# Optimization experiments

Measured on AMD Instinct MI355X. Metric: run time of the kernel, lower is better.

## Reference

```python
import jax, jax.numpy as jnp
import numpy as np
from jax import lax

B, H, W, C = 16, 32, 32, 256
HEADS = 8
HD = C // HEADS          # attention_head_dim = 32
KSZ = 3                  # conv_kernel_size
DIL = 2                  # dilation_rate
SCALE = HD ** -0.5


def setup_inputs() -> dict:
    key = jax.random.key(0)
    k0, k1, k2, k3 = jax.random.split(key, 4)
    return {
        "query": jax.random.normal(k0, (B, H, W, C), jnp.float32),
        "key_in": jax.random.normal(k1, (B, H, W, C), jnp.float32),
        "value": jax.random.normal(k2, (B, H, W, C), jnp.float32),
        # depthwise conv: kernel [kh, kw, in_ch/groups=1, out_ch=C], plus bias [C]
        "conv_kernel": jax.random.normal(k3, (KSZ, KSZ, 1, C), jnp.float32) * 0.05,
        "conv_bias": jnp.zeros((C,), jnp.float32),
    }


def _dwconv(x, kernel, bias):
    # depthwise dilated conv, padding SAME (Keras Conv2D groups=C)
    y = lax.conv_general_dilated(
        x, kernel,
        window_strides=(1, 1), padding="SAME",
        rhs_dilation=(DIL, DIL),
        dimension_numbers=("NHWC", "HWIO", "NHWC"),
        feature_group_count=C,
    )
    return y + bias


def _to_heads(x):
    # [B,H,W,C] -> [B, heads, S, head_dim]
    return x.reshape(B, H * W, HEADS, HD).transpose(0, 2, 1, 3)


def reference(query, key_in, value, conv_kernel, conv_bias):
    q = _to_heads(query)
    k = _to_heads(_dwconv(key_in, conv_kernel, conv_bias))
    v = _to_heads(_dwconv(value, conv_kernel, conv_bias))
    scores = jnp.einsum("bhqd,bhkd->bhqk", q, k) * SCALE  # [B,heads,S,S]
    attn = jax.nn.softmax(scores, axis=-1)
    out = jnp.einsum("bhqk,bhkd->bhqd", attn, v)          # [B,heads,S,hd]
    return out.transpose(0, 2, 1, 3).reshape(B, H, W, C)
```

## Files before the change

### kernel.cpp

```cpp
#include <hip/hip_runtime.h>

#define B_    16
#define HH    32
#define WW    32
#define CC    256
#define HEADS 8
#define HD    32
#define S_    1024
#define KT    128
#define NITER (S_ / KT)
#define SCALE_L2E 0.25503486f

typedef unsigned short u16;
typedef unsigned int   u32;
typedef __attribute__((ext_vector_type(8))) short short8;
typedef __attribute__((ext_vector_type(4))) float f32x4;

__device__ __forceinline__ u16 f2bf(float f) {
    u32 x = __float_as_uint(f);
    return (u16)((x + 0x7fffu + ((x >> 16) & 1u)) >> 16);
}
__device__ __forceinline__ u32 pack2bf(float lo, float hi) {
    return (u32)f2bf(lo) | ((u32)f2bf(hi) << 16);
}

#define GLD_LDS16(gp, lp)                                                 \
    __builtin_amdgcn_global_load_lds(                                     \
        (const __attribute__((address_space(1))) void*)(gp),              \
        (__attribute__((address_space(3))) void*)(lp), 16, 0, 0)

__global__ __launch_bounds__(256, 5) void dw_conv_kernel(
    const float* __restrict__ key_in, const float* __restrict__ value,
    const float* __restrict__ ck, const float* __restrict__ cb,
    u16* __restrict__ Kws, u16* __restrict__ Vws)
{
    __shared__ float4 tile[2048];

    const int tid = threadIdx.x;
    const int blk = blockIdx.x;
    const int g  = blk & 7;
    const int yt = (blk >> 3) & 7;
    const int b  = (blk >> 6) & 15;
    const int t  = blk >> 10;
    const float4* __restrict__ src4 = (const float4*)(t ? value : key_in);
    const int y0 = yt * 4;

    {
        const int x  = (tid >> 3) & 31;
        const int cc = tid & 7;
        #pragma unroll
        for (int i = 0; i < 8; i++) {
            int yy = y0 - 2 + i;
            if (yy >= 0 && yy < HH) {
                const float4* gp = src4 +
                    ((((size_t)b * HH + yy) * WW + x) * 64 + g * 8 + cc);
                GLD_LDS16(gp, &tile[tid + i * 256]);
            }
        }
    }

    const int c = tid & 7;
    float4 w9[9];
    #pragma unroll
    for (int j = 0; j < 9; j++)
        w9[j] = *(const float4*)(ck + j * CC + g * 32 + c * 4);
    const float4 bias = *(const float4*)(cb + g * 32 + c * 4);

    __syncthreads();

    #pragma unroll
    for (int i = 0; i < 4; i++) {
        int o = tid + i * 256;
        int x = (o >> 3) & 31;
        const int ry = i;
        float4 acc = bias;
        #pragma unroll
        for (int kh = 0; kh < 3; kh++) {
            int yy = y0 + ry - 2 + 2 * kh;
            if (yy < 0 || yy >= HH) continue;
            #pragma unroll
            for (int kw = 0; kw < 3; kw++) {
                int xx = x - 2 + 2 * kw;
                if (xx < 0 || xx >= WW) continue;
                float4 v = tile[((ry + 2 * kh) * 32 + xx) * 8 + c];
                float4 w = w9[kh * 3 + kw];
                acc.x += w.x * v.x; acc.y += w.y * v.y;
                acc.z += w.z * v.z; acc.w += w.w * v.w;
            }
        }
        int spix = (y0 + ry) * WW + x;
        size_t off = (((size_t)(b * HEADS + g)) * S_ + spix) * HD + c * 4;
        if (t == 0)
            *(uint2*)&Kws[off] = make_uint2(pack2bf(acc.x * SCALE_L2E, acc.y * SCALE_L2E),
                                            pack2bf(acc.z * SCALE_L2E, acc.w * SCALE_L2E));
        else
            *(uint2*)&Vws[off] = make_uint2(pack2bf(acc.x, acc.y), pack2bf(acc.z, acc.w));
    }
}

__global__ __launch_bounds__(256, 4) void attn_kernel(
    const float* __restrict__ query,
    const u16* __restrict__ Kws, const u16* __restrict__ Vws,
    float* __restrict__ out)
{
    __shared__ __align__(16) u16 Vtlds[2][HD][KT + 8];

    const int tid  = threadIdx.x;
    const int lane = tid & 63;
    const int wv   = tid >> 6;
    const int q15  = lane & 15;
    const int quad = lane >> 4;

    const int blk = blockIdx.x;
    const int bh  = blk & 127;
    const int qt  = blk >> 7;
    const int b = bh >> 3, h = bh & 7;
    const int q0w = qt * 128 + wv * 32;

    short8 qf[2];
    #pragma unroll
    for (int f = 0; f < 2; f++) {
        const float* qp = query + ((size_t)(b * S_ + q0w + f * 16 + q15)) * CC
                          + h * HD + quad * 8;
        float4 a = *(const float4*)(qp);
        float4 c = *(const float4*)(qp + 4);
        short8 v;
        v[0] = (short)f2bf(a.x); v[1] = (short)f2bf(a.y);
        v[2] = (short)f2bf(a.z); v[3] = (short)f2bf(a.w);
        v[4] = (short)f2bf(c.x); v[5] = (short)f2bf(c.y);
        v[6] = (short)f2bf(c.z); v[7] = (short)f2bf(c.w);
        qf[f] = v;
    }

    short8 ones;
    #pragma unroll
    for (int j = 0; j < 8; j++) ones[j] = (short)0x3F80;

    const u16* Kg = Kws + (size_t)bh * S_ * HD;
    const u16* Vg = Vws + (size_t)bh * S_ * HD;

    const int vg  = tid >> 3, vs4 = tid & 7;
    const int vc = vg >> 3, vw = vg & 7;
    const int vt2 = (vw >> 2) & 1, vqd = vw & 3;
    const int vpg = (vc << 5) | (vqd << 3) | (vt2 << 2);

    uint2 vr0, vr1, vr2, vr3;

    auto issue_v_loads = [&](int kt0) {
        const uint2* vsrc = (const uint2*)(Vg + (size_t)(kt0 + 4 * vg) * HD + 4 * vs4);
        vr0 = vsrc[0]; vr1 = vsrc[8]; vr2 = vsrc[16]; vr3 = vsrc[24];
    };
    auto write_lds = [&](int p) {
        u32 a, bb;
        a  = __builtin_amdgcn_perm(vr1.x, vr0.x, 0x05040100u);
        bb = __builtin_amdgcn_perm(vr3.x, vr2.x, 0x05040100u);
        *(uint2*)&Vtlds[p][4 * vs4 + 0][vpg] = make_uint2(a, bb);
        a  = __builtin_amdgcn_perm(vr1.x, vr0.x, 0x07060302u);
        bb = __builtin_amdgcn_perm(vr3.x, vr2.x, 0x07060302u);
        *(uint2*)&Vtlds[p][4 * vs4 + 1][vpg] = make_uint2(a, bb);
        a  = __builtin_amdgcn_perm(vr1.y, vr0.y, 0x05040100u);
        bb = __builtin_amdgcn_perm(vr3.y, vr2.y, 0x05040100u);
        *(uint2*)&Vtlds[p][4 * vs4 + 2][vpg] = make_uint2(a, bb);
        a  = __builtin_amdgcn_perm(vr1.y, vr0.y, 0x07060302u);
        bb = __builtin_amdgcn_perm(vr3.y, vr2.y, 0x07060302u);
        *(uint2*)&Vtlds[p][4 * vs4 + 3][vpg] = make_uint2(a, bb);
    };

    f32x4 Ot[2][2];
    f32x4 Dsum[2];
    #pragma unroll
    for (int f = 0; f < 2; f++) {
        Ot[f][0] = (f32x4)0.f; Ot[f][1] = (f32x4)0.f; Dsum[f] = (f32x4)0.f;
    }

    issue_v_loads(0);
    write_lds(0);

    for (int it = 0; it < NITER; it++) {
        const int p = it & 1;
        const int kt0 = it * KT;

        short8 kfr0[4], kfr1[4];
        #pragma unroll
        for (int c = 0; c < 4; c++) {
            kfr0[c] = *(const short8*)(Kg + (size_t)(kt0 + c * 32 + q15) * HD + quad * 8);
            kfr1[c] = *(const short8*)(Kg + (size_t)(kt0 + c * 32 + 16 + q15) * HD + quad * 8);
        }
        if (it + 1 < NITER) issue_v_loads((it + 1) * KT);
        __syncthreads();

        #pragma unroll
        for (int c = 0; c < 4; c++) {
            short8 vf0 = *(const short8*)&Vtlds[p][q15][c * 32 + quad * 8];
            short8 vf1 = *(const short8*)&Vtlds[p][16 + q15][c * 32 + quad * 8];
            #pragma unroll
            for (int f = 0; f < 2; f++) {
                f32x4 s0 = __builtin_amdgcn_mfma_f32_16x16x32_bf16(kfr0[c], qf[f], (f32x4)0.f, 0, 0, 0);
                f32x4 s1 = __builtin_amdgcn_mfma_f32_16x16x32_bf16(kfr1[c], qf[f], (f32x4)0.f, 0, 0, 0);
                #pragma unroll
                for (int r = 0; r < 4; r++) {
                    s0[r] = __builtin_amdgcn_exp2f(s0[r]);
                    s1[r] = __builtin_amdgcn_exp2f(s1[r]);
                }
                union { u32 u[4]; short8 s8; } pk;
                pk.u[0] = __builtin_amdgcn_perm(__float_as_uint(s0[1]),
                                                __float_as_uint(s0[0]), 0x07060302u);
                pk.u[1] = __builtin_amdgcn_perm(__float_as_uint(s0[3]),
                                                __float_as_uint(s0[2]), 0x07060302u);
                pk.u[2] = __builtin_amdgcn_perm(__float_as_uint(s1[1]),
                                                __float_as_uint(s1[0]), 0x07060302u);
                pk.u[3] = __builtin_amdgcn_perm(__float_as_uint(s1[3]),
                                                __float_as_uint(s1[2]), 0x07060302u);
                Ot[f][0] = __builtin_amdgcn_mfma_f32_16x16x32_bf16(vf0, pk.s8, Ot[f][0], 0, 0, 0);
                Ot[f][1] = __builtin_amdgcn_mfma_f32_16x16x32_bf16(vf1, pk.s8, Ot[f][1], 0, 0, 0);
                Dsum[f]  = __builtin_amdgcn_mfma_f32_16x16x32_bf16(ones, pk.s8, Dsum[f], 0, 0, 0);
            }
        }
        if (it + 1 < NITER) write_lds((it + 1) & 1);
    }

    #pragma unroll
    for (int f = 0; f < 2; f++) {
        float inv = 1.0f / Dsum[f][0];
        int qg = q0w + f * 16 + q15;
        float* op = out + ((size_t)(b * S_ + qg)) * CC + h * HD;
        #pragma unroll
        for (int h2 = 0; h2 < 2; h2++)
            #pragma unroll
            for (int r = 0; r < 4; r++)
                op[h2 * 16 + quad * 4 + r] = Ot[f][h2][r] * inv;
    }
}

extern "C" void kernel_launch(void* const* d_in, const int* in_sizes, int n_in,
                              void* d_out, int out_size, void* d_ws, size_t ws_size,
                              hipStream_t stream)
{
    const float* query  = (const float*)d_in[0];
    const float* key_in = (const float*)d_in[1];
    const float* value  = (const float*)d_in[2];
    const float* ck     = (const float*)d_in[3];
    const float* cb     = (const float*)d_in[4];
    float* out = (float*)d_out;

    u16* Kws = (u16*)d_ws;
    u16* Vws = Kws + (size_t)B_ * HEADS * S_ * HD;

    dw_conv_kernel<<<2048, 256, 0, stream>>>(
        key_in, value, ck, cb, Kws, Vws);

    attn_kernel<<<(B_ * HEADS * S_) / 128, 256, 0, stream>>>(
        query, Kws, Vws, out);
}
```

Before: 123.4 us.

## Make depthwise conv blocks process four row tiles with double-buffered async loads

The depthwise conv kernel now has each block handle four consecutive 4-row tiles instead of one, cutting the grid from 2048 to 512 blocks. Input rows are staged into two LDS buffers with asynchronous global-to-LDS loads, so loading the next tile overlaps with computing the current one. Manual vmcnt and lgkmcnt waits plus barriers replace the single __syncthreads. The aim is to hide load latency and amortise the weight and bias loads. The cost is doubled LDS per block and lower occupancy, and the conv is only a small share of the total run time next to the attention kernel.

```diff
diff --git a/kernel.cpp b/kernel.cpp
--- a/kernel.cpp
+++ b/kernel.cpp
@@ -29,35 +29,40 @@
         (const __attribute__((address_space(1))) void*)(gp),              \
         (__attribute__((address_space(3))) void*)(lp), 16, 0, 0)
 
-__global__ __launch_bounds__(256, 5) void dw_conv_kernel(
+__global__ __launch_bounds__(256, 2) void dw_conv_kernel(
     const float* __restrict__ key_in, const float* __restrict__ value,
     const float* __restrict__ ck, const float* __restrict__ cb,
     u16* __restrict__ Kws, u16* __restrict__ Vws)
 {
-    __shared__ float4 tile[2048];
+    __shared__ float4 tile[2][2048];
 
     const int tid = threadIdx.x;
     const int blk = blockIdx.x;
-    const int g  = blk & 7;
-    const int yt = (blk >> 3) & 7;
-    const int b  = (blk >> 6) & 15;
-    const int t  = blk >> 10;
+    const int g    = blk & 7;
+    const int half = (blk >> 3) & 1;
+    const int b    = (blk >> 4) & 15;
+    const int t    = blk >> 8;
     const float4* __restrict__ src4 = (const float4*)(t ? value : key_in);
-    const int y0 = yt * 4;
-
-    {
-        const int x  = (tid >> 3) & 31;
-        const int cc = tid & 7;
+    const int yt0 = half * 4;
+
+    const int xs = (tid >> 3) & 31;
+    const int cs = tid & 7;
+
+    auto stage = [&](int tl, int buf) {
+        const int y0 = (yt0 + tl) * 4;
         #pragma unroll
         for (int i = 0; i < 8; i++) {
             int yy = y0 - 2 + i;
             if (yy >= 0 && yy < HH) {
                 const float4* gp = src4 +
-                    ((((size_t)b * HH + yy) * WW + x) * 64 + g * 8 + cc);
-                GLD_LDS16(gp, &tile[tid + i * 256]);
+                    ((((size_t)b * HH + yy) * WW + xs) * 64 + g * 8 + cs);
+                GLD_LDS16(gp, &tile[buf][tid + i * 256]);
             }
         }
-    }
+    };
+
+    stage(0, 0);
+    stage(1, 1);
 
     const int c = tid & 7;
     float4 w9[9];
@@ -66,35 +71,49 @@
         w9[j] = *(const float4*)(ck + j * CC + g * 32 + c * 4);
     const float4 bias = *(const float4*)(cb + g * 32 + c * 4);
 
-    __syncthreads();
-
-    #pragma unroll
-    for (int i = 0; i < 4; i++) {
-        int o = tid + i * 256;
-        int x = (o >> 3) & 31;
-        const int ry = i;
-        float4 acc = bias;
-        #pragma unroll
-        for (int kh = 0; kh < 3; kh++) {
-            int yy = y0 + ry - 2 + 2 * kh;
-            if (yy < 0 || yy >= HH) continue;
+    #pragma unroll
+    for (int tl = 0; tl < 4; tl++) {
+        if (tl < 3) asm volatile("s_waitcnt vmcnt(8)" ::: "memory");
+        else        asm volatile("s_waitcnt vmcnt(0)" ::: "memory");
+        __builtin_amdgcn_s_barrier();
+        __builtin_amdgcn_sched_barrier(0);
+
+        const int y0  = (yt0 + tl) * 4;
+        const int buf = tl & 1;
+
+        #pragma unroll
+        for (int i = 0; i < 4; i++) {
+            int o = tid + i * 256;
+            int x = (o >> 3) & 31;
+            const int ry = i;
+            float4 acc = bias;
             #pragma unroll
-            for (int kw = 0; kw < 3; kw++) {
-                int xx = x - 2 + 2 * kw;
-                if (xx < 0 || xx >= WW) continue;
-                float4 v = tile[((ry + 2 * kh) * 32 + xx) * 8 + c];
-                float4 w = w9[kh * 3 + kw];
-                acc.x += w.x * v.x; acc.y += w.y * v.y;
-                acc.z += w.z * v.z; acc.w += w.w * v.w;
+            for (int kh = 0; kh < 3; kh++) {
+                int yy = y0 + ry - 2 + 2 * kh;
+                if (yy < 0 || yy >= HH) continue;
+                #pragma unroll
+                for (int kw = 0; kw < 3; kw++) {
+                    int xx = x - 2 + 2 * kw;
+                    if (xx < 0 || xx >= WW) continue;
+                    float4 v = tile[buf][((ry + 2 * kh) * 32 + xx) * 8 + c];
+                    float4 w = w9[kh * 3 + kw];
+                    acc.x += w.x * v.x; acc.y += w.y * v.y;
+                    acc.z += w.z * v.z; acc.w += w.w * v.w;
+                }
             }
-        }
-        int spix = (y0 + ry) * WW + x;
-        size_t off = (((size_t)(b * HEADS + g)) * S_ + spix) * HD + c * 4;
-        if (t == 0)
-            *(uint2*)&Kws[off] = make_uint2(pack2bf(acc.x * SCALE_L2E, acc.y * SCALE_L2E),
-                                            pack2bf(acc.z * SCALE_L2E, acc.w * SCALE_L2E));
-        else
-            *(uint2*)&Vws[off] = make_uint2(pack2bf(acc.x, acc.y), pack2bf(acc.z, acc.w));
+            int spix = (y0 + ry) * WW + x;
+            size_t off = (((size_t)(b * HEADS + g)) * S_ + spix) * HD + c * 4;
+            if (t == 0)
+                *(uint2*)&Kws[off] = make_uint2(pack2bf(acc.x * SCALE_L2E, acc.y * SCALE_L2E),
+                                                pack2bf(acc.z * SCALE_L2E, acc.w * SCALE_L2E));
+            else
+                *(uint2*)&Vws[off] = make_uint2(pack2bf(acc.x, acc.y), pack2bf(acc.z, acc.w));
+        }
+
+        asm volatile("s_waitcnt lgkmcnt(0)" ::: "memory");
+        __builtin_amdgcn_s_barrier();
+        __builtin_amdgcn_sched_barrier(0);
+        if (tl + 2 < 4) stage(tl + 2, tl & 1);
     }
 }
 
@@ -246,7 +265,7 @@
     u16* Kws = (u16*)d_ws;
     u16* Vws = Kws + (size_t)B_ * HEADS * S_ * HD;
 
-    dw_conv_kernel<<<2048, 256, 0, stream>>>(
+    dw_conv_kernel<<<512, 256, 0, stream>>>(
         key_in, value, ck, cb, Kws, Vws);
 
     attn_kernel<<<(B_ * HEADS * S_) / 128, 256, 0, stream>>>(
```

Measured after the change: 126.0 us. +2.1%, slower.
